# Optimization experiments

Measured on AMD Instinct MI355X. Metric: run time of the kernel, lower is better.

## Reference

```python
import jax, jax.numpy as jnp
import numpy as np

D = 768
H = 8
HD = D // H
MLP = 3072
EPS = 1e-5


def _ln(x, g, b):
    mu = jnp.mean(x, axis=-1, keepdims=True)
    var = jnp.var(x, axis=-1, keepdims=True)
    return (x - mu) * jax.lax.rsqrt(var + EPS) * g + b


def setup_inputs() -> dict:
    key = jax.random.key(0)
    ks = jax.random.split(key, 20)
    B, N = 4, 2048
    s = 0.02
    inp = {
        "x": jax.random.normal(ks[0], (B, N, D), jnp.float32),
        "position_bias": jax.random.normal(ks[1], (N, N), jnp.float32),
        "wq": jax.random.normal(ks[2], (D, D), jnp.float32) * s,
        "bq": jnp.zeros((D,), jnp.float32),
        "wk": jax.random.normal(ks[3], (D, D), jnp.float32) * s,
        "bk": jnp.zeros((D,), jnp.float32),
        "wv": jax.random.normal(ks[4], (D, D), jnp.float32) * s,
        "bv": jnp.zeros((D,), jnp.float32),
        "wo": jax.random.normal(ks[5], (D, D), jnp.float32) * s,
        "bo": jnp.zeros((D,), jnp.float32),
        "g1": jnp.ones((D,), jnp.float32),
        "b1": jnp.zeros((D,), jnp.float32),
        "g2": jnp.ones((D,), jnp.float32),
        "b2": jnp.zeros((D,), jnp.float32),
        "w_ff1": jax.random.normal(ks[6], (D, MLP), jnp.float32) * s,
        "b_ff1": jnp.zeros((MLP,), jnp.float32),
        "w_ff2": jax.random.normal(ks[7], (MLP, D), jnp.float32) * s,
        "b_ff2": jnp.zeros((D,), jnp.float32),
    }
    return inp


def reference(x, position_bias, wq, bq, wk, bk, wv, bv, wo, bo, g1, b1, g2, b2, w_ff1, b_ff1, w_ff2, b_ff2):
    B, N, _ = x.shape
    scale = HD ** -0.5
    # pre-norm attention
    n1 = _ln(x, g1, b1)
    q = (n1 @ wq + bq).reshape(B, N, H, HD).transpose(0, 2, 1, 3)
    k = (n1 @ wk + bk).reshape(B, N, H, HD).transpose(0, 2, 1, 3)
    v = (n1 @ wv + bv).reshape(B, N, H, HD).transpose(0, 2, 1, 3)
    attn = jnp.einsum('bhqd,bhkd->bhqk', q, k) * scale  # [B,H,N,N]
    attn = attn + position_bias[None, None, :, :]
    attn = jax.nn.softmax(attn, axis=-1)
    out = jnp.einsum('bhqk,bhkd->bhqd', attn, v)
    out = out.transpose(0, 2, 1, 3).reshape(B, N, D)
    out = out @ wo + bo
    x = x + out
    # pre-norm GELU MLP (exact erf gelu, torch default)
    n2 = _ln(x, g2, b2)
    h = jax.nn.gelu(n2 @ w_ff1 + b_ff1, approximate=False)
    x = x + (h @ w_ff2 + b_ff2)
    return x
```

## Files before the change

### kernel.cpp

```cpp
#include <hip/hip_runtime.h>
#include <hip/hip_bf16.h>

#define D 768
#define H 8
#define HD 96
#define MLP 3072
#define NB 2048
#define BATCH 4

typedef __attribute__((ext_vector_type(8))) short short8;
typedef __attribute__((ext_vector_type(4))) short short4v;
typedef __attribute__((ext_vector_type(4))) float f32x4;

typedef const __attribute__((address_space(1))) unsigned int gu32;
typedef __attribute__((address_space(3))) unsigned int lu32;

__device__ inline void gload16(const void* g, void* l){
  __builtin_amdgcn_global_load_lds((gu32*)g, (lu32*)l, 16, 0, 0);
}

__device__ inline short f2b(float f){
  __hip_bfloat16 h = __float2bfloat16(f);
  return *reinterpret_cast<short*>(&h);
}
__device__ inline float b2f(short s){
  return __uint_as_float(((unsigned)(unsigned short)s) << 16);
}
__device__ inline float fexp2(float x){ return __builtin_amdgcn_exp2f(x); }

__global__ __launch_bounds__(256) void wtrans(const float* __restrict__ in, short* __restrict__ out, int K, int Nc){
  __shared__ float tile[32][33];
  int bk = blockIdx.x, bn = blockIdx.y;
  int tx = threadIdx.x & 31, ty = threadIdx.x >> 5;
  #pragma unroll
  for (int i=0;i<4;++i)
    tile[ty + i*8][tx] = in[(size_t)(bk*32 + ty + i*8)*Nc + bn*32 + tx];
  __syncthreads();
  #pragma unroll
  for (int i=0;i<4;++i)
    out[(size_t)(bn*32 + ty + i*8)*K + bk*32 + tx] = f2b(tile[tx][ty + i*8]);
}

__global__ __launch_bounds__(256) void bias_cat(const float* __restrict__ bq, const float* __restrict__ bk,
                                                const float* __restrict__ bv, float* __restrict__ o){
  int i = blockIdx.x*256 + threadIdx.x;
  if (i < 768){ o[i]=bq[i]; o[768+i]=bk[i]; o[1536+i]=bv[i]; }
}

__global__ __launch_bounds__(256) void cvt_pb(const float* __restrict__ in, short* __restrict__ out){
  int i = blockIdx.x*256 + threadIdx.x;
  const float L2E = 1.4426950408889634f;
  f32x4 v = *(const f32x4*)&in[(size_t)i*4];
  short4v o;
  o[0]=f2b(v[0]*L2E); o[1]=f2b(v[1]*L2E); o[2]=f2b(v[2]*L2E); o[3]=f2b(v[3]*L2E);
  *(short4v*)&out[(size_t)i*4] = o;
}

__global__ __launch_bounds__(256) void ln_k(const float* __restrict__ X, const float* __restrict__ gg,
                                            const float* __restrict__ bb, short* __restrict__ out){
  int row = blockIdx.x, t = threadIdx.x;
  const float* x = X + (size_t)row*D;
  float v0=x[t], v1=x[t+256], v2=x[t+512];
  float s=v0+v1+v2, ss=v0*v0+v1*v1+v2*v2;
  #pragma unroll
  for (int m=1;m<64;m<<=1){ s += __shfl_xor(s,m); ss += __shfl_xor(ss,m); }
  __shared__ float red[8];
  int w=t>>6, lane=t&63;
  if (!lane){ red[w]=s; red[4+w]=ss; }
  __syncthreads();
  s = red[0]+red[1]+red[2]+red[3];
  ss = red[4]+red[5]+red[6]+red[7];
  float mu = s*(1.f/768.f);
  float inv = rsqrtf(ss*(1.f/768.f) - mu*mu + 1e-5f);
  short* o = out + (size_t)row*D;
  o[t]     = f2b((v0-mu)*inv*gg[t]     + bb[t]);
  o[t+256] = f2b((v1-mu)*inv*gg[t+256] + bb[t+256]);
  o[t+512] = f2b((v2-mu)*inv*gg[t+512] + bb[t+512]);
}

template<int MODE>
__global__ __launch_bounds__(256) void gemm_bt(
    const short* __restrict__ A, const short* __restrict__ Bt,
    const float* __restrict__ bias, const float* __restrict__ resid,
    void* __restrict__ Cout, int Nc, int K)
{
  __shared__ __align__(16) short As[128][32];
  __shared__ __align__(16) short Bs[128][32];
  int m0 = blockIdx.x*128, n0 = blockIdx.y*128;
  int t = threadIdx.x;
  int lane = t & 63, w = t >> 6;
  int wm = w >> 1, wn = w & 1;
  int r = lane & 15, g = lane >> 4;
  const short* aSrc = A  + (size_t)(m0 + (t>>2))*K + (t&3)*8;
  const short* bSrc = Bt + (size_t)(n0 + (t>>2))*K + (t&3)*8;
  char* aDst0 = (char*)As + w*1024;
  char* aDst1 = (char*)As + 4096 + w*1024;
  char* bDst0 = (char*)Bs + w*1024;
  char* bDst1 = (char*)Bs + 4096 + w*1024;
  size_t rowK64 = (size_t)64*K;
  f32x4 acc[4][4] = {};
  for (int kt=0; kt<K; kt+=32){
    gload16(aSrc + kt,          aDst0);
    gload16(aSrc + kt + rowK64, aDst1);
    gload16(bSrc + kt,          bDst0);
    gload16(bSrc + kt + rowK64, bDst1);
    __syncthreads();
    short8 af[4], bfr[4];
    #pragma unroll
    for (int i=0;i<4;++i){
      af[i]  = *(const short8*)&As[wm*64 + i*16 + r][g*8];
      bfr[i] = *(const short8*)&Bs[wn*64 + i*16 + r][g*8];
    }
    #pragma unroll
    for (int i=0;i<4;++i)
      #pragma unroll
      for (int j=0;j<4;++j)
        acc[i][j] = __builtin_amdgcn_mfma_f32_16x16x32_bf16(af[i], bfr[j], acc[i][j], 0,0,0);
    __syncthreads();
  }
  #pragma unroll
  for (int i=0;i<4;++i){
    #pragma unroll
    for (int j=0;j<4;++j){
      int col = n0 + wn*64 + j*16 + r;
      float bv = bias[col];
      #pragma unroll
      for (int q=0;q<4;++q){
        int row = m0 + wm*64 + i*16 + g*4 + q;
        size_t idx = (size_t)row*Nc + col;
        float val = acc[i][j][q] + bv;
        if constexpr (MODE==0){
          ((short*)Cout)[idx] = f2b(val);
        } else if constexpr (MODE==2){
          float ge = 0.5f*val*(1.f + erff(val*0.70710678118654752f));
          ((short*)Cout)[idx] = f2b(ge);
        }
      }
    }
  }
}

template<int MODE>
__global__ __launch_bounds__(256) void gemm64(
    const short* __restrict__ A, const short* __restrict__ Bt,
    const float* __restrict__ bias, const float* __restrict__ resid,
    void* __restrict__ Cout, int Nc, int K)
{
  __shared__ __align__(16) short As[64][32];
  __shared__ __align__(16) short Bs[128][32];
  int m0 = blockIdx.x*64, n0 = blockIdx.y*128;
  int t = threadIdx.x;
  int lane = t & 63, w = t >> 6;
  int r = lane & 15, g = lane >> 4;
  const short* aSrc = A  + (size_t)(m0 + (t>>2))*K + (t&3)*8;
  const short* bSrc = Bt + (size_t)(n0 + (t>>2))*K + (t&3)*8;
  char* aDst  = (char*)As + w*1024;
  char* bDst0 = (char*)Bs + w*1024;
  char* bDst1 = (char*)Bs + 4096 + w*1024;
  size_t rowK64 = (size_t)64*K;
  f32x4 acc[4][2] = {};
  for (int kt=0; kt<K; kt+=32){
    gload16(aSrc + kt,          aDst);
    gload16(bSrc + kt,          bDst0);
    gload16(bSrc + kt + rowK64, bDst1);
    __syncthreads();
    short8 af[4], bfr[2];
    #pragma unroll
    for (int i=0;i<4;++i) af[i] = *(const short8*)&As[i*16 + r][g*8];
    #pragma unroll
    for (int j=0;j<2;++j) bfr[j] = *(const short8*)&Bs[w*32 + j*16 + r][g*8];
    #pragma unroll
    for (int i=0;i<4;++i)
      #pragma unroll
      for (int j=0;j<2;++j)
        acc[i][j] = __builtin_amdgcn_mfma_f32_16x16x32_bf16(af[i], bfr[j], acc[i][j], 0,0,0);
    __syncthreads();
  }
  #pragma unroll
  for (int i=0;i<4;++i){
    #pragma unroll
    for (int j=0;j<2;++j){
      int col = n0 + w*32 + j*16 + r;
      #pragma unroll
      for (int q=0;q<4;++q){
        int row = m0 + i*16 + g*4 + q;
        if constexpr (MODE==1){
          size_t idx = (size_t)row*Nc + col;
          ((float*)Cout)[idx] = acc[i][j][q] + bias[col] + resid[idx];
        } else {
          int hh = row / 96, hd = row - hh*96;
          int bb = col >> 11, nn = col & 2047;
          size_t idx = ((size_t)((bb*8 + hh)*96 + hd))*2048 + nn;
          ((short*)Cout)[idx] = f2b(acc[i][j][q] + bias[row]);
        }
      }
    }
  }
}

__global__ __launch_bounds__(512, 4) void attn_k(const short* __restrict__ qkv, const short* __restrict__ v_t,
                                                 const short* __restrict__ pb, short* __restrict__ aout){
  int bx = blockIdx.x;
  int qb = bx & 15, h = (bx>>4)&7, b = bx>>7;
  int t = threadIdx.x, lane = t&63, w = t>>6;
  int r = lane&15, g = lane>>4;
  __shared__ __align__(16) short Ks[2][64][96];
  __shared__ __align__(16) short Vs[96][64];
  __shared__ __align__(16) short Ps[8][16][72];
  const float SCALE2 = 0.10206207261596575f * 1.4426950408889634f;
  short8 qa[3];
  #pragma unroll
  for (int ks=0;ks<3;++ks)
    qa[ks] = *(const short8*)&qkv[(size_t)(b*NB + qb*128 + w*16 + r)*1536 + h*HD + ks*32 + g*8];
  f32x4 oacc[6] = {};
  float m_run[4], l_run[4];
  #pragma unroll
  for (int j=0;j<4;++j){ m_run[j] = -1e30f; l_run[j] = 0.f; }
  const short* pbbase = pb + (size_t)(qb*128 + w*16 + g*4)*NB + r;
  int kc1row = t/12,       kc1off = (t%12)*8;
  int kc2row = (512+t)/12, kc2off = ((512+t)%12)*8;
  int vrow1 = t>>3,        voff1 = ((t&7) ^ (vrow1&7))*8;
  int vrow2 = (512+t)>>3,  voff2 = (((512+t)&7) ^ (vrow2&7))*8;
  const short* kg = qkv + (size_t)(b*NB)*1536 + 768 + h*HD;
  const short* vg = v_t + (size_t)((b*H+h)*HD)*NB;
  bool wlow = (w < 4);
  gload16(kg + (size_t)kc1row*1536 + kc1off, (char*)Ks + w*1024);
  if (wlow) gload16(kg + (size_t)kc2row*1536 + kc2off, (char*)Ks + 8192 + w*1024);
  int cur = 0;
  for (int kt=0; kt<32; ++kt){
    int kbase = kt*64;
    __syncthreads();
    float pbv[4][4];
    #pragma unroll
    for (int j=0;j<4;++j)
      #pragma unroll
      for (int n=0;n<4;++n)
        pbv[j][n] = b2f(pbbase[(size_t)j*NB + kbase + n*16]);
    if (kt < 31){
      const short* kgn = kg + (size_t)(kbase+64)*1536;
      char* kd = (char*)Ks + (cur^1)*12288;
      gload16(kgn + (size_t)kc1row*1536 + kc1off, kd + w*1024);
      if (wlow) gload16(kgn + (size_t)kc2row*1536 + kc2off, kd + 8192 + w*1024);
    }
    gload16(vg + (size_t)vrow1*NB + kbase + voff1, (char*)Vs + w*1024);
    if (wlow) gload16(vg + (size_t)vrow2*NB + kbase + voff2, (char*)Vs + 8192 + w*1024);
    f32x4 sacc[4] = {};
    __builtin_amdgcn_s_setprio(1);
    #pragma unroll
    for (int ks=0;ks<3;++ks){
      short8 kb[4];
      #pragma unroll
      for (int n=0;n<4;++n) kb[n] = *(const short8*)&Ks[cur][n*16 + r][ks*32 + g*8];
      #pragma unroll
      for (int n=0;n<4;++n)
        sacc[n] = __builtin_amdgcn_mfma_f32_16x16x32_bf16(qa[ks], kb[n], sacc[n], 0,0,0);
    }
    __builtin_amdgcn_s_setprio(0);
    float vals[4][4], pmax[4];
    #pragma unroll
    for (int j=0;j<4;++j){
      #pragma unroll
      for (int n=0;n<4;++n)
        vals[j][n] = fmaf(sacc[n][j], SCALE2, pbv[j][n]);
      float pm = fmaxf(fmaxf(vals[j][0],vals[j][1]), fmaxf(vals[j][2],vals[j][3]));
      pm = fmaxf(pm, __shfl_xor(pm,1));
      pm = fmaxf(pm, __shfl_xor(pm,2));
      pm = fmaxf(pm, __shfl_xor(pm,4));
      pm = fmaxf(pm, __shfl_xor(pm,8));
      pmax[j] = pm;
    }
    float need = pmax[0]-m_run[0];
    need = fmaxf(need, pmax[1]-m_run[1]);
    need = fmaxf(need, pmax[2]-m_run[2]);
    need = fmaxf(need, pmax[3]-m_run[3]);
    if (__any(need > 8.f)){
      #pragma unroll
      for (int j=0;j<4;++j){
        float mn = fmaxf(m_run[j], pmax[j]);
        float f = fexp2(m_run[j] - mn);
        l_run[j] *= f; m_run[j] = mn;
        #pragma unroll
        for (int n=0;n<6;++n) oacc[n][j] *= f;
      }
    }
    #pragma unroll
    for (int j=0;j<4;++j){
      float rs = 0.f;
      #pragma unroll
      for (int n=0;n<4;++n){
        float pe = fexp2(vals[j][n] - m_run[j]);
        rs += pe;
        Ps[w][g*4 + j][n*16 + r] = f2b(pe);
      }
      rs += __shfl_xor(rs,1); rs += __shfl_xor(rs,2);
      rs += __shfl_xor(rs,4); rs += __shfl_xor(rs,8);
      l_run[j] += rs;
    }
    asm volatile("s_waitcnt vmcnt(0)" ::: "memory");
    __builtin_amdgcn_s_setprio(1);
    #pragma unroll
    for (int ks2=0;ks2<2;++ks2){
      short8 pa = *(const short8*)&Ps[w][r][ks2*32 + g*8];
      #pragma unroll
      for (int n=0;n<6;++n){
        short8 vb = *(const short8*)&Vs[n*16 + r][((ks2*4 + g) ^ (r&7))*8];
        oacc[n] = __builtin_amdgcn_mfma_f32_16x16x32_bf16(pa, vb, oacc[n], 0,0,0);
      }
    }
    __builtin_amdgcn_s_setprio(0);
    cur ^= 1;
  }
  #pragma unroll
  for (int j=0;j<4;++j){
    float inv = 1.f / l_run[j];
    #pragma unroll
    for (int n=0;n<6;++n){
      int rowg = b*NB + qb*128 + w*16 + g*4 + j;
      int col = h*HD + n*16 + r;
      aout[(size_t)rowg*D + col] = f2b(oacc[n][j]*inv);
    }
  }
}

extern "C" void kernel_launch(void* const* d_in, const int* in_sizes, int n_in,
                              void* d_out, int out_size, void* d_ws, size_t ws_size,
                              hipStream_t stream){
  const float* x   = (const float*)d_in[0];
  const float* pb  = (const float*)d_in[1];
  const float* wq  = (const float*)d_in[2];
  const float* bq  = (const float*)d_in[3];
  const float* wk  = (const float*)d_in[4];
  const float* bk  = (const float*)d_in[5];
  const float* wv  = (const float*)d_in[6];
  const float* bv  = (const float*)d_in[7];
  const float* wo  = (const float*)d_in[8];
  const float* bo  = (const float*)d_in[9];
  const float* g1  = (const float*)d_in[10];
  const float* b1  = (const float*)d_in[11];
  const float* g2  = (const float*)d_in[12];
  const float* b2  = (const float*)d_in[13];
  const float* wf1 = (const float*)d_in[14];
  const float* bf1 = (const float*)d_in[15];
  const float* wf2 = (const float*)d_in[16];
  const float* bf2 = (const float*)d_in[17];
  float* out = (float*)d_out;

  char* p = (char*)d_ws;
  auto alloc = [&](size_t bytes){ char* q = p; p += (bytes + 255) & ~(size_t)255; return q; };
  short* wqkv_t = (short*)alloc((size_t)2304*768*2);
  short* wo_t   = (short*)alloc((size_t)768*768*2);
  short* w1_t   = (short*)alloc((size_t)3072*768*2);
  short* w2_t   = (short*)alloc((size_t)768*3072*2);
  float* bqkv   = (float*)alloc(2304*4);
  short* pb16   = (short*)alloc((size_t)2048*2048*2);
  float* x1     = (float*)alloc((size_t)8192*768*4);
  short* n2     = (short*)alloc((size_t)8192*768*2);
  short* n1     = (short*)alloc((size_t)8192*768*2);
  short* qkv    = (short*)alloc((size_t)8192*1536*2);
  short* v_t    = (short*)alloc((size_t)32*96*2048*2);
  short* hbuf   = n1;
  short* attn_o = n1;
  short* wv_t   = wqkv_t + (size_t)2*768*768;

  wtrans<<<dim3(24,24),256,0,stream>>>(wq, wqkv_t,           768, 768);
  wtrans<<<dim3(24,24),256,0,stream>>>(wk, wqkv_t + 768*768, 768, 768);
  wtrans<<<dim3(24,24),256,0,stream>>>(wv, wv_t,             768, 768);
  wtrans<<<dim3(24,24),256,0,stream>>>(wo, wo_t, 768, 768);
  wtrans<<<dim3(24,96),256,0,stream>>>(wf1, w1_t, 768, 3072);
  wtrans<<<dim3(96,24),256,0,stream>>>(wf2, w2_t, 3072, 768);
  bias_cat<<<3,256,0,stream>>>(bq,bk,bv,bqkv);
  cvt_pb<<<4096,256,0,stream>>>(pb, pb16);
  ln_k<<<8192,256,0,stream>>>(x, g1, b1, n1);
  gemm_bt<0><<<dim3(64,12),256,0,stream>>>(n1, wqkv_t, bqkv, nullptr, qkv, 1536, 768);
  gemm64<5><<<dim3(12,64),256,0,stream>>>(wv_t, n1, bv, nullptr, v_t, 0, 768);
  attn_k<<<512,512,0,stream>>>(qkv, v_t, pb16, attn_o);
  gemm64<1><<<dim3(128,6),256,0,stream>>>(attn_o, wo_t, bo, x, x1, 768, 768);
  ln_k<<<8192,256,0,stream>>>(x1, g2, b2, n2);
  gemm_bt<2><<<dim3(64,24),256,0,stream>>>(n2, w1_t, bf1, nullptr, hbuf, 3072, 768);
  gemm64<1><<<dim3(128,6),256,0,stream>>>(hbuf, w2_t, bf2, x1, out, 768, 3072);
}
```

Before: 372.9 us.

## Rewrite attention with 32x32 MFMA, register-resident P and pre-tiled position bias

Rebuilds the attention kernel around 32x32x16 bf16 MFMAs computing S^T, so each lane owns one query column and the softmax row max and sum need only a single cross-half shuffle. P is packed to bf16 in registers with v_cvt_pk and lane swaps, so the LDS round trip through Ps goes away. Position bias is pre-permuted into a per-lane fragment layout, so each lane reads contiguous 16-byte chunks instead of scattered scalars. Blocks now cover 256 queries (256 blocks at occupancy 1), K is staged through registers into a swizzled LDS tile, and there is an extra barrier per step. The larger tiles and lower occupancy risk latency stalls and leave fewer blocks than before to fill the GPU.

```diff
diff --git a/kernel.cpp b/kernel.cpp
--- a/kernel.cpp
+++ b/kernel.cpp
@@ -11,6 +11,8 @@
 typedef __attribute__((ext_vector_type(8))) short short8;
 typedef __attribute__((ext_vector_type(4))) short short4v;
 typedef __attribute__((ext_vector_type(4))) float f32x4;
+typedef __attribute__((ext_vector_type(16))) float f32x16;
+typedef __attribute__((ext_vector_type(4))) int int4v;
 
 typedef const __attribute__((address_space(1))) unsigned int gu32;
 typedef __attribute__((address_space(3))) unsigned int lu32;
@@ -27,6 +29,12 @@
   return __uint_as_float(((unsigned)(unsigned short)s) << 16);
 }
 __device__ inline float fexp2(float x){ return __builtin_amdgcn_exp2f(x); }
+
+__device__ inline unsigned cvtpk(float lo, float hi){
+  unsigned r;
+  asm volatile("v_cvt_pk_bf16_f32 %0, %1, %2" : "=v"(r) : "v"(lo), "v"(hi));
+  return r;
+}
 
 __global__ __launch_bounds__(256) void wtrans(const float* __restrict__ in, short* __restrict__ out, int K, int Nc){
   __shared__ float tile[32][33];
@@ -47,13 +55,23 @@
   if (i < 768){ o[i]=bq[i]; o[768+i]=bk[i]; o[1536+i]=bv[i]; }
 }
 
-__global__ __launch_bounds__(256) void cvt_pb(const float* __restrict__ in, short* __restrict__ out){
-  int i = blockIdx.x*256 + threadIdx.x;
+__global__ __launch_bounds__(256) void pb_reorg(const float* __restrict__ pb, short* __restrict__ pbT){
+  int qt = blockIdx.x, kb = blockIdx.y;
+  int t = threadIdx.x;
+  int l = t >> 2;
+  int vbase = (t & 3) * 8;
+  int q = qt*32 + (l & 31);
+  int hi = l >> 5;
   const float L2E = 1.4426950408889634f;
-  f32x4 v = *(const f32x4*)&in[(size_t)i*4];
-  short4v o;
-  o[0]=f2b(v[0]*L2E); o[1]=f2b(v[1]*L2E); o[2]=f2b(v[2]*L2E); o[3]=f2b(v[3]*L2E);
-  *(short4v*)&out[(size_t)i*4] = o;
+  short8 o;
+  #pragma unroll
+  for (int j=0;j<8;++j){
+    int v = vbase + j;
+    int r = v & 15, tile = v >> 4;
+    int k = kb*64 + tile*32 + 8*(r>>2) + (r&3) + 4*hi;
+    o[j] = f2b(pb[(size_t)q*NB + k] * L2E);
+  }
+  *(short8*)&pbT[(((size_t)(qt*32 + kb))*64 + l)*32 + vbase] = o;
 }
 
 __global__ __launch_bounds__(256) void ln_k(const float* __restrict__ X, const float* __restrict__ gg,
@@ -198,126 +216,172 @@
   }
 }
 
-__global__ __launch_bounds__(512, 4) void attn_k(const short* __restrict__ qkv, const short* __restrict__ v_t,
-                                                 const short* __restrict__ pb, short* __restrict__ aout){
+__global__ __launch_bounds__(512, 1) void attn_k(const short* __restrict__ qkv, const short* __restrict__ v_t,
+                                                 const short* __restrict__ pbT, short* __restrict__ aout){
   int bx = blockIdx.x;
-  int qb = bx & 15, h = (bx>>4)&7, b = bx>>7;
-  int t = threadIdx.x, lane = t&63, w = t>>6;
-  int r = lane&15, g = lane>>4;
-  __shared__ __align__(16) short Ks[2][64][96];
+  int h = bx & 7, b = (bx>>3)&3, qb = bx>>5;
+  int t = threadIdx.x, l = t & 63, w = t >> 6;
+  int l31 = l & 31, hi = l >> 5, l7 = l & 7;
+  __shared__ __align__(16) short Ks[2][64][128];
   __shared__ __align__(16) short Vs[96][64];
-  __shared__ __align__(16) short Ps[8][16][72];
   const float SCALE2 = 0.10206207261596575f * 1.4426950408889634f;
-  short8 qa[3];
-  #pragma unroll
-  for (int ks=0;ks<3;++ks)
-    qa[ks] = *(const short8*)&qkv[(size_t)(b*NB + qb*128 + w*16 + r)*1536 + h*HD + ks*32 + g*8];
-  f32x4 oacc[6] = {};
-  float m_run[4], l_run[4];
-  #pragma unroll
-  for (int j=0;j<4;++j){ m_run[j] = -1e30f; l_run[j] = 0.f; }
-  const short* pbbase = pb + (size_t)(qb*128 + w*16 + g*4)*NB + r;
-  int kc1row = t/12,       kc1off = (t%12)*8;
-  int kc2row = (512+t)/12, kc2off = ((512+t)%12)*8;
-  int vrow1 = t>>3,        voff1 = ((t&7) ^ (vrow1&7))*8;
-  int vrow2 = (512+t)>>3,  voff2 = (((512+t)&7) ^ (vrow2&7))*8;
-  const short* kg = qkv + (size_t)(b*NB)*1536 + 768 + h*HD;
-  const short* vg = v_t + (size_t)((b*H+h)*HD)*NB;
-  bool wlow = (w < 4);
-  gload16(kg + (size_t)kc1row*1536 + kc1off, (char*)Ks + w*1024);
-  if (wlow) gload16(kg + (size_t)kc2row*1536 + kc2off, (char*)Ks + 8192 + w*1024);
-  int cur = 0;
+
+  int qRow = qb*256 + w*32 + l31;
+  const short* qg = qkv + (size_t)(b*NB + qRow)*1536 + h*HD;
+  short8 qa[6];
+  #pragma unroll
+  for (int ds=0; ds<6; ++ds)
+    qa[ds] = *(const short8*)&qg[ds*16 + hi*8];
+
+  f32x16 oacc[3] = {};
+  float m_run = -3.0e38f, l_run = 0.f;
+
+  int r0 = t/12,        c0 = t%12;
+  int s1 = 512 + t;
+  int r1 = s1/12,       c1 = s1%12;
+  int ldsK0 = r0*128 + (c0 ^ (r0&7))*8;
+  int ldsK1 = r1*128 + (c1 ^ (r1&7))*8;
+  const short* kgB = qkv + (size_t)(b*NB)*1536 + 768 + h*HD;
+  bool wlow = (t < 256);
+  int vr0 = t>>3,  vc0 = t&7;
+  int vr1 = (512+t)>>3, vc1 = (512+t)&7;
+  const short* vgB = v_t + (size_t)((b*H+h)*HD)*NB;
+  const short* vsrc0 = vgB + (size_t)vr0*NB + (vc0 ^ (vr0&7))*8;
+  const short* vsrc1 = vgB + (size_t)vr1*NB + (vc1 ^ (vr1&7))*8;
+  char* vdst0 = (char*)Vs + w*1024;
+  char* vdst1 = (char*)Vs + 8192 + w*1024;
+  const short* pbB = pbT + (((size_t)((qb*8 + w)*32))*64 + l)*32;
+
+  {
+    short8 ka = *(const short8*)&kgB[(size_t)r0*1536 + c0*8];
+    short* ks0 = &Ks[0][0][0];
+    *(short8*)(ks0 + ldsK0) = ka;
+    if (wlow){
+      short8 kb = *(const short8*)&kgB[(size_t)r1*1536 + c1*8];
+      *(short8*)(ks0 + ldsK1) = kb;
+    }
+  }
+  __syncthreads();
+
   for (int kt=0; kt<32; ++kt){
+    int cur = kt & 1;
     int kbase = kt*64;
+    const short* pbk = pbB + kt*2048;
+    short8 pbr0 = *(const short8*)&pbk[0];
+    short8 pbr1 = *(const short8*)&pbk[8];
+    short8 pbr2 = *(const short8*)&pbk[16];
+    short8 pbr3 = *(const short8*)&pbk[24];
+    gload16(vsrc0 + kbase, vdst0);
+    if (wlow) gload16(vsrc1 + kbase, vdst1);
+    int kb2 = (kt < 31) ? (kbase + 64) : kbase;
+    short8 kra = *(const short8*)&kgB[(size_t)(kb2 + r0)*1536 + c0*8];
+    short8 krb = {};
+    if (wlow) krb = *(const short8*)&kgB[(size_t)(kb2 + r1)*1536 + c1*8];
+
+    f32x16 sacc[2] = {};
+    __builtin_amdgcn_s_setprio(1);
+    #pragma unroll
+    for (int tt=0; tt<2; ++tt){
+      #pragma unroll
+      for (int ds=0; ds<6; ++ds){
+        short8 kf = *(const short8*)&Ks[cur][tt*32 + l31][((ds*2 + hi) ^ l7)*8];
+        sacc[tt] = __builtin_amdgcn_mfma_f32_32x32x16_bf16(kf, qa[ds], sacc[tt], 0,0,0);
+      }
+    }
+    __builtin_amdgcn_s_setprio(0);
+
+    float vals[2][16];
+    #pragma unroll
+    for (int tt=0; tt<2; ++tt)
+      #pragma unroll
+      for (int r=0; r<16; ++r){
+        int v = tt*16 + r;
+        short pv = (v<8)?pbr0[v]:(v<16)?pbr1[v-8]:(v<24)?pbr2[v-16]:pbr3[v-24];
+        vals[tt][r] = fmaf(sacc[tt][r], SCALE2, b2f(pv));
+      }
+    float pm = vals[0][0];
+    #pragma unroll
+    for (int tt=0; tt<2; ++tt)
+      #pragma unroll
+      for (int r=0; r<16; ++r) pm = fmaxf(pm, vals[tt][r]);
+    pm = fmaxf(pm, __shfl_xor(pm, 32));
+    if (__any(pm - m_run > 8.f)){
+      float mn = fmaxf(m_run, pm);
+      float f = fexp2(m_run - mn);
+      l_run *= f; m_run = mn;
+      int fi = __float_as_int(f);
+      #pragma unroll
+      for (int reg=0; reg<16; ++reg){
+        int q = (reg&3) + 8*(reg>>2) + 4*hi;
+        float fr = __int_as_float(__builtin_amdgcn_ds_bpermute(q<<2, fi));
+        oacc[0][reg] *= fr; oacc[1][reg] *= fr; oacc[2][reg] *= fr;
+      }
+    }
+    float p[2][16];
+    float rs = 0.f;
+    #pragma unroll
+    for (int tt=0; tt<2; ++tt)
+      #pragma unroll
+      for (int r=0; r<16; ++r){
+        p[tt][r] = fexp2(vals[tt][r] - m_run);
+        rs += p[tt][r];
+      }
+    rs += __shfl_xor(rs, 32);
+    l_run += rs;
+
+    short8 pa[4];
+    #pragma unroll
+    for (int ks=0; ks<4; ++ks){
+      int tt = ks>>1;
+      int rb = (ks&1)*8;
+      unsigned G0a = cvtpk(p[tt][rb+0], p[tt][rb+1]);
+      unsigned G0b = cvtpk(p[tt][rb+2], p[tt][rb+3]);
+      unsigned G1a = cvtpk(p[tt][rb+4], p[tt][rb+5]);
+      unsigned G1b = cvtpk(p[tt][rb+6], p[tt][rb+7]);
+      unsigned sG0a = (unsigned)__shfl_xor((int)G0a, 32);
+      unsigned sG0b = (unsigned)__shfl_xor((int)G0b, 32);
+      unsigned sG1a = (unsigned)__shfl_xor((int)G1a, 32);
+      unsigned sG1b = (unsigned)__shfl_xor((int)G1b, 32);
+      int4v wv;
+      wv[0] = hi ? (int)sG1a : (int)G0a;
+      wv[1] = hi ? (int)sG1b : (int)G0b;
+      wv[2] = hi ? (int)G1a  : (int)sG0a;
+      wv[3] = hi ? (int)G1b  : (int)sG0b;
+      pa[ks] = __builtin_bit_cast(short8, wv);
+    }
+
     __syncthreads();
-    float pbv[4][4];
-    #pragma unroll
-    for (int j=0;j<4;++j)
-      #pragma unroll
-      for (int n=0;n<4;++n)
-        pbv[j][n] = b2f(pbbase[(size_t)j*NB + kbase + n*16]);
+
+    __builtin_amdgcn_s_setprio(1);
+    #pragma unroll
+    for (int dt=0; dt<3; ++dt){
+      #pragma unroll
+      for (int ks=0; ks<4; ++ks){
+        short8 vb = *(const short8*)&Vs[dt*32 + l31][((ks*2 + hi) ^ l7)*8];
+        oacc[dt] = __builtin_amdgcn_mfma_f32_32x32x16_bf16(pa[ks], vb, oacc[dt], 0,0,0);
+      }
+    }
+    __builtin_amdgcn_s_setprio(0);
+
     if (kt < 31){
-      const short* kgn = kg + (size_t)(kbase+64)*1536;
-      char* kd = (char*)Ks + (cur^1)*12288;
-      gload16(kgn + (size_t)kc1row*1536 + kc1off, kd + w*1024);
-      if (wlow) gload16(kgn + (size_t)kc2row*1536 + kc2off, kd + 8192 + w*1024);
-    }
-    gload16(vg + (size_t)vrow1*NB + kbase + voff1, (char*)Vs + w*1024);
-    if (wlow) gload16(vg + (size_t)vrow2*NB + kbase + voff2, (char*)Vs + 8192 + w*1024);
-    f32x4 sacc[4] = {};
-    __builtin_amdgcn_s_setprio(1);
-    #pragma unroll
-    for (int ks=0;ks<3;++ks){
-      short8 kb[4];
-      #pragma unroll
-      for (int n=0;n<4;++n) kb[n] = *(const short8*)&Ks[cur][n*16 + r][ks*32 + g*8];
-      #pragma unroll
-      for (int n=0;n<4;++n)
-        sacc[n] = __builtin_amdgcn_mfma_f32_16x16x32_bf16(qa[ks], kb[n], sacc[n], 0,0,0);
-    }
-    __builtin_amdgcn_s_setprio(0);
-    float vals[4][4], pmax[4];
-    #pragma unroll
-    for (int j=0;j<4;++j){
-      #pragma unroll
-      for (int n=0;n<4;++n)
-        vals[j][n] = fmaf(sacc[n][j], SCALE2, pbv[j][n]);
-      float pm = fmaxf(fmaxf(vals[j][0],vals[j][1]), fmaxf(vals[j][2],vals[j][3]));
-      pm = fmaxf(pm, __shfl_xor(pm,1));
-      pm = fmaxf(pm, __shfl_xor(pm,2));
-      pm = fmaxf(pm, __shfl_xor(pm,4));
-      pm = fmaxf(pm, __shfl_xor(pm,8));
-      pmax[j] = pm;
-    }
-    float need = pmax[0]-m_run[0];
-    need = fmaxf(need, pmax[1]-m_run[1]);
-    need = fmaxf(need, pmax[2]-m_run[2]);
-    need = fmaxf(need, pmax[3]-m_run[3]);
-    if (__any(need > 8.f)){
-      #pragma unroll
-      for (int j=0;j<4;++j){
-        float mn = fmaxf(m_run[j], pmax[j]);
-        float f = fexp2(m_run[j] - mn);
-        l_run[j] *= f; m_run[j] = mn;
-        #pragma unroll
-        for (int n=0;n<6;++n) oacc[n][j] *= f;
-      }
-    }
-    #pragma unroll
-    for (int j=0;j<4;++j){
-      float rs = 0.f;
-      #pragma unroll
-      for (int n=0;n<4;++n){
-        float pe = fexp2(vals[j][n] - m_run[j]);
-        rs += pe;
-        Ps[w][g*4 + j][n*16 + r] = f2b(pe);
-      }
-      rs += __shfl_xor(rs,1); rs += __shfl_xor(rs,2);
-      rs += __shfl_xor(rs,4); rs += __shfl_xor(rs,8);
-      l_run[j] += rs;
-    }
-    asm volatile("s_waitcnt vmcnt(0)" ::: "memory");
-    __builtin_amdgcn_s_setprio(1);
-    #pragma unroll
-    for (int ks2=0;ks2<2;++ks2){
-      short8 pa = *(const short8*)&Ps[w][r][ks2*32 + g*8];
-      #pragma unroll
-      for (int n=0;n<6;++n){
-        short8 vb = *(const short8*)&Vs[n*16 + r][((ks2*4 + g) ^ (r&7))*8];
-        oacc[n] = __builtin_amdgcn_mfma_f32_16x16x32_bf16(pa, vb, oacc[n], 0,0,0);
-      }
-    }
-    __builtin_amdgcn_s_setprio(0);
-    cur ^= 1;
-  }
-  #pragma unroll
-  for (int j=0;j<4;++j){
-    float inv = 1.f / l_run[j];
-    #pragma unroll
-    for (int n=0;n<6;++n){
-      int rowg = b*NB + qb*128 + w*16 + g*4 + j;
-      int col = h*HD + n*16 + r;
-      aout[(size_t)rowg*D + col] = f2b(oacc[n][j]*inv);
+      short* ksn = &Ks[cur^1][0][0];
+      *(short8*)(ksn + ldsK0) = kra;
+      if (wlow) *(short8*)(ksn + ldsK1) = krb;
+      __syncthreads();
+    }
+  }
+
+  float inv_self = 1.f / l_run;
+  int ii = __float_as_int(inv_self);
+  #pragma unroll
+  for (int reg=0; reg<16; ++reg){
+    int q = (reg&3) + 8*(reg>>2) + 4*hi;
+    float invq = __int_as_float(__builtin_amdgcn_ds_bpermute(q<<2, ii));
+    int rowg = b*NB + qb*256 + w*32 + q;
+    #pragma unroll
+    for (int dt=0; dt<3; ++dt){
+      int col = h*HD + dt*32 + l31;
+      aout[(size_t)rowg*D + col] = f2b(oacc[dt][reg] * invq);
     }
   }
 }
@@ -352,7 +416,7 @@
   short* w1_t   = (short*)alloc((size_t)3072*768*2);
   short* w2_t   = (short*)alloc((size_t)768*3072*2);
   float* bqkv   = (float*)alloc(2304*4);
-  short* pb16   = (short*)alloc((size_t)2048*2048*2);
+  short* pbT    = (short*)alloc((size_t)2048*2048*2);
   float* x1     = (float*)alloc((size_t)8192*768*4);
   short* n2     = (short*)alloc((size_t)8192*768*2);
   short* n1     = (short*)alloc((size_t)8192*768*2);
@@ -369,11 +433,11 @@
   wtrans<<<dim3(24,96),256,0,stream>>>(wf1, w1_t, 768, 3072);
   wtrans<<<dim3(96,24),256,0,stream>>>(wf2, w2_t, 3072, 768);
   bias_cat<<<3,256,0,stream>>>(bq,bk,bv,bqkv);
-  cvt_pb<<<4096,256,0,stream>>>(pb, pb16);
+  pb_reorg<<<dim3(64,32),256,0,stream>>>(pb, pbT);
   ln_k<<<8192,256,0,stream>>>(x, g1, b1, n1);
   gemm_bt<0><<<dim3(64,12),256,0,stream>>>(n1, wqkv_t, bqkv, nullptr, qkv, 1536, 768);
   gemm64<5><<<dim3(12,64),256,0,stream>>>(wv_t, n1, bv, nullptr, v_t, 0, 768);
-  attn_k<<<512,512,0,stream>>>(qkv, v_t, pb16, attn_o);
+  attn_k<<<256,512,0,stream>>>(qkv, v_t, pbT, attn_o);
   gemm64<1><<<dim3(128,6),256,0,stream>>>(attn_o, wo_t, bo, x, x1, 768, 768);
   ln_k<<<8192,256,0,stream>>>(x1, g2, b2, n2);
   gemm_bt<2><<<dim3(64,24),256,0,stream>>>(n2, w1_t, bf1, nullptr, hbuf, 3072, 768);
```

New measurement: 338.4 us. 1.1x faster.
